# Performance work log

Measured on AMD Instinct MI355X. Metric: run time of the kernel, lower is better.

The kernel has to match this reference:

```python
import jax, jax.numpy as jnp
import numpy as np

B, N, C = 8, 4096, 1024
H = 16
D = C // H  # head_dim = 64
SCALE = D ** -0.5


def setup_inputs() -> dict:
    key = jax.random.key(0)
    ks = jax.random.split(key, 5)
    std = C ** -0.5
    return {
        "x": jax.random.normal(ks[0], (B, N, C), dtype=jnp.float32),
        "Wq": jax.random.normal(ks[1], (C, C), dtype=jnp.float32) * std,
        "Wk": jax.random.normal(ks[2], (C, C), dtype=jnp.float32) * std,
        "Wv": jax.random.normal(ks[3], (C, C), dtype=jnp.float32) * std,
        "Wo": jax.random.normal(ks[4], (C, C), dtype=jnp.float32) * std,
        "bo": jnp.zeros((C,), dtype=jnp.float32),
    }


def reference(x, Wq, Wk, Wv, Wo, bo):
    b, n, c = x.shape
    # projections -> (B, N, H, D)
    q = (x @ Wq).reshape(b, n, H, D)
    k = (x @ Wk).reshape(b, n, H, D)
    v = (x @ Wv).reshape(b, n, H, D)
    # feature maps: softmax over head_dim for q, over sequence for k
    q = jax.nn.softmax(q, axis=-1) * SCALE
    k = jax.nn.softmax(k, axis=1)
    # O(N) linear attention: kv summary then apply to q
    kv = jnp.einsum("bnhf,bnhd->bhfd", k, v)   # (B, H, D, D)
    y = jnp.einsum("bnhf,bhfd->bnhd", q, kv)   # (B, N, H, D)
    y = y.reshape(b, n, H * D)
    return y @ Wo + bo
```

## Files before the change

### kernel.cpp

```cpp
#include <hip/hip_runtime.h>


typedef unsigned short u16;
typedef __bf16 bf16x8v __attribute__((ext_vector_type(8)));
typedef float f32x4 __attribute__((ext_vector_type(4)));
typedef u16 u16x8 __attribute__((ext_vector_type(8)));
typedef u16 u16x4 __attribute__((ext_vector_type(4)));

#define AS1C(p) (const __attribute__((address_space(1))) void*)(p)
#define AS3(p)  (__attribute__((address_space(3))) void*)(p)

__device__ __forceinline__ float b2f(u16 u) {
    union { unsigned u; float f; } c; c.u = ((unsigned)u) << 16; return c.f;
}
__device__ __forceinline__ u16 f2b(float f) {
    union { float f; unsigned u; } c; c.f = f;
    unsigned x = c.u + 0x7fffu + ((c.u >> 16) & 1u);
    return (u16)(x >> 16);
}

__global__ void prep(const float* __restrict__ x, u16* __restrict__ xb,
                     const float* __restrict__ Wq, const float* __restrict__ Wk,
                     const float* __restrict__ Wv, const float* __restrict__ Wo,
                     u16* __restrict__ wt, u16* __restrict__ wot) {
    if (blockIdx.x < 1024) {
        __shared__ float tl[64][65];
        const int which = blockIdx.x >> 8;
        const float* src = which == 0 ? Wq : which == 1 ? Wk : which == 2 ? Wv : Wo;
        u16* dst = which < 3 ? wt + which * 1048576 : wot;
        const int bx = blockIdx.x & 255;
        const int tx = bx & 15, ty = bx >> 4;
        const int j = threadIdx.x & 63, i0 = threadIdx.x >> 6;
        #pragma unroll
        for (int it = 0; it < 16; ++it) {
            int i = it * 4 + i0;
            tl[i][j] = src[(ty * 64 + i) * 1024 + tx * 64 + j];
        }
        __syncthreads();
        #pragma unroll
        for (int it = 0; it < 16; ++it) {
            int i = it * 4 + i0;
            dst[(tx * 64 + i) * 1024 + ty * 64 + j] = f2b(tl[j][i]);
        }
    } else {
        const long n4 = 8388608L;
        long i = (long)(blockIdx.x - 1024) * blockDim.x + threadIdx.x;
        long stride = 2048L * blockDim.x;
        for (long jj = i; jj < n4; jj += stride) {
            float4 v = ((const float4*)x)[jj];
            u16x4 o = { f2b(v.x), f2b(v.y), f2b(v.z), f2b(v.w) };
            ((u16x4*)xb)[jj] = o;
        }
    }
}

template<int OUTMODE>
__global__ __launch_bounds__(512, 2) void gemm256(
    const u16* __restrict__ A, const u16* __restrict__ Bt,
    void* __restrict__ Cout, const float* __restrict__ bias,
    const int lda, const int ldc, const int ntn, const int nwg, const long btBatch)
{
    __shared__ __align__(16) u16 lds[65536];
    const int t = threadIdx.x;
    const int w = t >> 6, lane = t & 63;
    const int l16 = lane & 15, g = lane >> 4;
    const int wr = w >> 2, wc = w & 3;

    const int cpx = nwg >> 3;
    const int bid = blockIdx.x;
    const int swzb = (bid & 7) * cpx + (bid >> 3);
    const int tm = swzb / ntn, tn = swzb - tm * ntn;
    const long row0 = (long)tm << 8, col0 = (long)tn << 8;
    const u16* BtB = Bt + (row0 >> 12) * btBatch;

    const int eo = (((t & 7) ^ ((t >> 3) & 7)) << 3);
    const u16* pA = A + (row0 + (t >> 3)) * (long)lda + eo;
    const u16* pB = BtB + (col0 + (t >> 3)) * 1024L + eo;
    const long a64 = (long)lda << 6;

#define STG_A(Tt, j) __builtin_amdgcn_global_load_lds(                        \
    AS1C(pA + (long)(j) * a64 + ((long)(Tt) << 6)),                           \
    AS3(lds + ((((Tt) & 1) << 15) + ((j) << 12) + t * 8)), 16, 0, 0);
#define STG_B(Tt, j) __builtin_amdgcn_global_load_lds(                        \
    AS1C(pB + (long)(j) * 65536L + ((long)(Tt) << 6)),                        \
    AS3(lds + ((((Tt) & 1) << 15) + 16384 + ((j) << 12) + t * 8)), 16, 0, 0);

    const int swz = l16 & 7;
    const int koff0 = ((0 * 4 + g) ^ swz) << 3;
    const int koff1 = ((1 * 4 + g) ^ swz) << 3;
    const int arow = ((wr << 7) + l16) << 6;
    const int brow = 16384 + (((wc << 6) + l16) << 6);

    u16x8 aM[4][2], b0[2][2], b1[2][2];
    f32x4 acc[8][4] = {};

#define RD_A(half) { _Pragma("unroll") for (int mi = 0; mi < 4; ++mi) {       \
    const int ab = bufE + arow + ((half) * 64 + mi * 16) * 64;                \
    aM[mi][0] = *(const u16x8*)&lds[ab + koff0];                              \
    aM[mi][1] = *(const u16x8*)&lds[ab + koff1]; } }
#define RD_B(nh, br) { _Pragma("unroll") for (int ni = 0; ni < 2; ++ni) {     \
    const int bb = bufE + brow + ((nh) * 32 + ni * 16) * 64;                  \
    br[ni][0] = *(const u16x8*)&lds[bb + koff0];                              \
    br[ni][1] = *(const u16x8*)&lds[bb + koff1]; } }
#define MM(mh, nh, br) { __builtin_amdgcn_s_setprio(1);                       \
    _Pragma("unroll") for (int mi = 0; mi < 4; ++mi)                          \
    { _Pragma("unroll") for (int ni = 0; ni < 2; ++ni) {                      \
    f32x4 c = acc[(mh)*4 + mi][(nh)*2 + ni];                                  \
    c = __builtin_amdgcn_mfma_f32_16x16x32_bf16(                              \
        __builtin_bit_cast(bf16x8v, aM[mi][0]),                               \
        __builtin_bit_cast(bf16x8v, br[ni][0]), c, 0, 0, 0);                  \
    c = __builtin_amdgcn_mfma_f32_16x16x32_bf16(                              \
        __builtin_bit_cast(bf16x8v, aM[mi][1]),                               \
        __builtin_bit_cast(bf16x8v, br[ni][1]), c, 0, 0, 0);                  \
    acc[(mh)*4 + mi][(nh)*2 + ni] = c; } }                                    \
    __builtin_amdgcn_s_setprio(0); }

    STG_A(0, 0) STG_A(0, 2) STG_B(0, 0) STG_B(0, 1)
    STG_B(0, 2) STG_B(0, 3) STG_A(0, 1) STG_A(0, 3)
    STG_A(1, 0) STG_A(1, 2) STG_B(1, 0) STG_B(1, 1)
    asm volatile("s_waitcnt vmcnt(6)" ::: "memory");
    __builtin_amdgcn_s_barrier();

    #pragma unroll 2
    for (int T = 0; T < 16; ++T) {
        const int bufE = (T & 1) << 15;
        RD_A(0) RD_B(0, b0)
        STG_B(T + 1, 2) STG_B(T + 1, 3)
        __builtin_amdgcn_s_barrier();
        MM(0, 0, b0)
        RD_B(1, b1)
        STG_A(T + 1, 1) STG_A(T + 1, 3)
        asm volatile("s_waitcnt vmcnt(8)" ::: "memory");
        __builtin_amdgcn_s_barrier();
        MM(0, 1, b1)
        RD_A(1)
        STG_A(T + 2, 0) STG_A(T + 2, 2)
        __builtin_amdgcn_s_barrier();
        MM(1, 0, b0)
        STG_B(T + 2, 0) STG_B(T + 2, 1)
        asm volatile("s_waitcnt vmcnt(6)" ::: "memory");
        __builtin_amdgcn_s_barrier();
        MM(1, 1, b1)
    }
    asm volatile("s_waitcnt vmcnt(0)" ::: "memory");
#undef STG_A
#undef STG_B
#undef RD_A
#undef RD_B
#undef MM

    if (OUTMODE == 2 && tn < 4) {
        #pragma unroll
        for (int mi = 0; mi < 8; ++mi) {
            #pragma unroll
            for (int r = 0; r < 4; ++r) {
                float v0 = acc[mi][0][r], v1 = acc[mi][1][r];
                float v2 = acc[mi][2][r], v3 = acc[mi][3][r];
                float m = fmaxf(fmaxf(v0, v1), fmaxf(v2, v3));
                m = fmaxf(m, __shfl_xor(m, 1)); m = fmaxf(m, __shfl_xor(m, 2));
                m = fmaxf(m, __shfl_xor(m, 4)); m = fmaxf(m, __shfl_xor(m, 8));
                v0 = __expf(v0 - m); v1 = __expf(v1 - m);
                v2 = __expf(v2 - m); v3 = __expf(v3 - m);
                float s = v0 + v1 + v2 + v3;
                s += __shfl_xor(s, 1); s += __shfl_xor(s, 2);
                s += __shfl_xor(s, 4); s += __shfl_xor(s, 8);
                const float sc = 0.125f / s;
                acc[mi][0][r] = v0 * sc; acc[mi][1][r] = v1 * sc;
                acc[mi][2][r] = v2 * sc; acc[mi][3][r] = v3 * sc;
            }
        }
    }
    if (OUTMODE == 2 && tn >= 4 && tn < 8) {
        #pragma unroll
        for (int mi = 0; mi < 8; ++mi)
            #pragma unroll
            for (int ni = 0; ni < 4; ++ni)
                #pragma unroll
                for (int r = 0; r < 4; ++r)
                    acc[mi][ni][r] = __expf(acc[mi][ni][r]);
    }

    const long crow = row0 + wr * 128 + g * 4;
    const long ccol = col0 + wc * 64 + l16;
    if (OUTMODE != 1) {
        u16* Cb = (u16*)Cout;
        #pragma unroll
        for (int mi = 0; mi < 8; ++mi) {
            #pragma unroll
            for (int ni = 0; ni < 4; ++ni) {
                long base = (crow + mi * 16) * (long)ldc + ccol + ni * 16;
                #pragma unroll
                for (int r = 0; r < 4; ++r)
                    Cb[base + (long)r * ldc] = f2b(acc[mi][ni][r]);
            }
        }
    } else {
        float* Cf = (float*)Cout;
        float bv[4];
        #pragma unroll
        for (int ni = 0; ni < 4; ++ni) bv[ni] = bias[ccol + ni * 16];
        #pragma unroll
        for (int mi = 0; mi < 8; ++mi) {
            #pragma unroll
            for (int ni = 0; ni < 4; ++ni) {
                long base = (crow + mi * 16) * (long)ldc + ccol + ni * 16;
                #pragma unroll
                for (int r = 0; r < 4; ++r)
                    Cf[base + (long)r * ldc] = acc[mi][ni][r] + bv[ni];
            }
        }
    }
}

__global__ __launch_bounds__(256) void kv_mfma(const u16* __restrict__ qkv,
                                               float* __restrict__ kvp,
                                               float* __restrict__ psum) {
    __shared__ __align__(16) u16 eT[64 * 72];
    __shared__ __align__(16) u16 vT[64 * 72];
    __shared__ float csb[256 * 8];
    const int t = threadIdx.x;
    const int bx = blockIdx.x;
    const int nc = bx & 15, h = (bx >> 4) & 15, b = bx >> 8;
    const int r = t >> 3;
    const int c = t & 7;
    const long rowbase = (long)b * 4096 + nc * 256;
    const u16* eg = qkv + (rowbase + r) * 3072 + 1024 + h * 64 + c * 8;
    const u16* vg = eg + 1024;
    const int w = t >> 6, lane = t & 63;
    const int l16 = lane & 15, g = lane >> 4;

    float cs[8] = {};
    f32x4 acc[4] = {};

    int aoff[2], boff[4][2];
    #pragma unroll
    for (int ks = 0; ks < 2; ++ks) {
        const int f = w * 16 + l16;
        aoff[ks] = f * 72 + ((ks * 32 + g * 8) ^ (((f >> 3) & 7) << 3));
        #pragma unroll
        for (int db = 0; db < 4; ++db) {
            const int d = db * 16 + l16;
            boff[db][ks] = d * 72 + ((ks * 32 + g * 8) ^ (((d >> 3) & 7) << 3));
        }
    }

    for (int n0 = 0; n0 < 256; n0 += 64) {
        const long go = (long)n0 * 3072;
        u16x8 e0 = *(const u16x8*)(eg + go);
        u16x8 e1 = *(const u16x8*)(eg + go + 32L * 3072);
        u16x8 v0 = *(const u16x8*)(vg + go);
        u16x8 v1 = *(const u16x8*)(vg + go + 32L * 3072);
        #pragma unroll
        for (int j = 0; j < 8; ++j) {
            cs[j] += b2f(e0[j]) + b2f(e1[j]);
            const int f = c * 8 + j;
            const int sw = ((f >> 3) & 7) << 3;
            eT[f * 72 + (r ^ sw)]        = e0[j];
            eT[f * 72 + ((r + 32) ^ sw)] = e1[j];
            vT[f * 72 + (r ^ sw)]        = v0[j];
            vT[f * 72 + ((r + 32) ^ sw)] = v1[j];
        }
        __syncthreads();
        #pragma unroll
        for (int ks = 0; ks < 2; ++ks) {
            bf16x8v af = __builtin_bit_cast(bf16x8v, *(const u16x8*)&eT[aoff[ks]]);
            #pragma unroll
            for (int db = 0; db < 4; ++db) {
                bf16x8v bf = __builtin_bit_cast(bf16x8v, *(const u16x8*)&vT[boff[db][ks]]);
                acc[db] = __builtin_amdgcn_mfma_f32_16x16x32_bf16(af, bf, acc[db], 0, 0, 0);
            }
        }
        __syncthreads();
    }

    float* o = kvp + (long)nc * 524288 + ((long)(b * 16 + h)) * 4096;
    #pragma unroll
    for (int db = 0; db < 4; ++db) {
        #pragma unroll
        for (int rr = 0; rr < 4; ++rr)
            o[(w * 16 + g * 4 + rr) * 64 + db * 16 + l16] = acc[db][rr];
    }

    #pragma unroll
    for (int j = 0; j < 8; ++j) csb[t * 8 + j] = cs[j];
    __syncthreads();
    if (t < 64) {
        const int cc = t >> 3, jj = t & 7;
        float s = 0.f;
        #pragma unroll 8
        for (int rr = 0; rr < 32; ++rr) s += csb[(cc + 8 * rr) * 8 + jj];
        psum[((long)nc * 128 + b * 16 + h) * 64 + t] = s;
    }
}

__global__ void kv_scale(const float* __restrict__ kvp, const float* __restrict__ psum,
                         u16* __restrict__ kvNb) {
    __shared__ float inv_s[64];
    const int bh = blockIdx.x;
    const int t = threadIdx.x;
    if (t < 64) {
        float s = 0.f;
        #pragma unroll
        for (int nc = 0; nc < 16; ++nc) s += psum[((long)nc * 128 + bh) * 64 + t];
        inv_s[t] = 1.0f / s;
    }
    __syncthreads();
    const float* p = kvp + (long)bh * 4096;
    u16* o = kvNb + (long)bh * 4096;
    const float inv = inv_s[t >> 2];
    #pragma unroll
    for (int j = 0; j < 4; ++j) {
        const int idx = t * 16 + j * 4;
        f32x4 v = {};
        #pragma unroll
        for (int nc = 0; nc < 16; ++nc) {
            f32x4 pv = *(const f32x4*)&p[(long)nc * 524288 + idx];
            #pragma unroll
            for (int e = 0; e < 4; ++e) v[e] += pv[e];
        }
        u16x4 ov = { f2b(v[0] * inv), f2b(v[1] * inv), f2b(v[2] * inv), f2b(v[3] * inv) };
        *(u16x4*)&o[idx] = ov;
    }
}

__global__ __launch_bounds__(256) void w2t_mfma(const u16* __restrict__ wot,
                                                const u16* __restrict__ kvNb,
                                                u16* __restrict__ w2t) {
    __shared__ __align__(16) u16 Qs[8192];
    const int t = threadIdx.x;
    const int bx = blockIdx.x;
    const int mt = bx & 7, h = (bx >> 3) & 15, b = bx >> 7;
    const int c0 = mt * 128;
    const int wave = t >> 6, lane = t & 63;
    const int wr = wave >> 1, wc = wave & 1;
    const int l16 = lane & 15, g = lane >> 4;

    const int colg = t & 7;
    const int rloc = t >> 3;
    #pragma unroll
    for (int p = 0; p < 4; ++p) {
        const int row = p * 32 + rloc;
        u16x8 qv = *(const u16x8*)(wot + (long)(c0 + row) * 1024 + h * 64 + colg * 8);
        const int chunk = colg ^ (row & 7);
        *(u16x8*)&Qs[row * 64 + chunk * 8] = qv;
    }
    __syncthreads();

    const u16* kvb = kvNb + ((long)(b * 16 + h) << 12);
    bf16x8v bkv[2][2];
    #pragma unroll
    for (int ni = 0; ni < 2; ++ni) {
        #pragma unroll
        for (int ks = 0; ks < 2; ++ks)
            bkv[ni][ks] = __builtin_bit_cast(bf16x8v,
                *(const u16x8*)(kvb + (wc * 32 + ni * 16 + l16) * 64 + ks * 32 + g * 8));
    }
    bf16x8v aq[4][2];
    #pragma unroll
    for (int mi = 0; mi < 4; ++mi) {
        const int row = wr * 64 + mi * 16 + l16;
        #pragma unroll
        for (int ks = 0; ks < 2; ++ks) {
            const int c16 = (ks * 4 + g) ^ (row & 7);
            aq[mi][ks] = __builtin_bit_cast(bf16x8v,
                *(const u16x8*)&Qs[row * 64 + c16 * 8]);
        }
    }
    f32x4 acc[4][2] = {};
    #pragma unroll
    for (int mi = 0; mi < 4; ++mi) {
        #pragma unroll
        for (int ni = 0; ni < 2; ++ni) {
            acc[mi][ni] = __builtin_amdgcn_mfma_f32_16x16x32_bf16(
                aq[mi][0], bkv[ni][0], acc[mi][ni], 0, 0, 0);
            acc[mi][ni] = __builtin_amdgcn_mfma_f32_16x16x32_bf16(
                aq[mi][1], bkv[ni][1], acc[mi][ni], 0, 0, 0);
        }
    }
    u16* ob = w2t + (long)b * 1048576;
    #pragma unroll
    for (int mi = 0; mi < 4; ++mi) {
        #pragma unroll
        for (int ni = 0; ni < 2; ++ni) {
            int row = c0 + wr * 64 + mi * 16 + g * 4;
            int col = h * 64 + wc * 32 + ni * 16 + l16;
            #pragma unroll
            for (int r = 0; r < 4; ++r)
                ob[(long)(row + r) * 1024 + col] = f2b(acc[mi][ni][r]);
        }
    }
}

extern "C" void kernel_launch(void* const* d_in, const int* in_sizes, int n_in,
                              void* d_out, int out_size, void* d_ws, size_t ws_size,
                              hipStream_t stream) {
    (void)in_sizes; (void)n_in; (void)out_size; (void)ws_size;
    const float* x  = (const float*)d_in[0];
    const float* Wq = (const float*)d_in[1];
    const float* Wk = (const float*)d_in[2];
    const float* Wv = (const float*)d_in[3];
    const float* Wo = (const float*)d_in[4];
    const float* bo = (const float*)d_in[5];

    u16* xb  = (u16*)d_ws;
    u16* wt  = xb + 33554432;
    u16* wot = wt + 3145728;
    u16* qkv = wot + 1048576;
    u16* kvNb = qkv + 100663296;
    float* kvp  = (float*)xb;
    float* psum = kvp + 8388608;
    u16* w2t = (u16*)(psum + 131072);

    prep<<<3072, 256, 0, stream>>>(x, xb, Wq, Wk, Wv, Wo, wt, wot);
    gemm256<2><<<1536, 512, 0, stream>>>(xb, wt, (void*)qkv, nullptr, 1024, 3072, 12, 1536, 0L);
    kv_mfma<<<2048, 256, 0, stream>>>(qkv, kvp, psum);
    kv_scale<<<128, 256, 0, stream>>>(kvp, psum, kvNb);
    w2t_mfma<<<1024, 256, 0, stream>>>(wot, kvNb, w2t);
    gemm256<1><<<512, 512, 0, stream>>>(qkv, w2t, d_out, bo, 3072, 1024, 4, 512, 1048576L);
}
```

Measured before the change: 359.9 us.

## Fuse KV-summary computation into QKV projection GEMM epilogue

Reorders the K and V weight columns so each 256-wide output tile holds K and V for two heads. The QKV GEMM epilogue then computes exp(K), the per-chunk column sums and the K^T V partial products with MFMA through LDS. Only Q is written to global memory, which removes the K/V store plus the separate kv_mfma pass that read them back. The cost is a heavier epilogue with extra LDS round trips and barriers inside the GEMM kernel.

```diff
diff --git a/kernel.cpp b/kernel.cpp
--- a/kernel.cpp
+++ b/kernel.cpp
@@ -27,7 +27,6 @@
         __shared__ float tl[64][65];
         const int which = blockIdx.x >> 8;
         const float* src = which == 0 ? Wq : which == 1 ? Wk : which == 2 ? Wv : Wo;
-        u16* dst = which < 3 ? wt + which * 1048576 : wot;
         const int bx = blockIdx.x & 255;
         const int tx = bx & 15, ty = bx >> 4;
         const int j = threadIdx.x & 63, i0 = threadIdx.x >> 6;
@@ -40,7 +39,12 @@
         #pragma unroll
         for (int it = 0; it < 16; ++it) {
             int i = it * 4 + i0;
-            dst[(tx * 64 + i) * 1024 + ty * 64 + j] = f2b(tl[j][i]);
+            long row;
+            u16* base;
+            if (which == 0)      { base = wt;  row = tx * 64 + i; }
+            else if (which == 3) { base = wot; row = tx * 64 + i; }
+            else                 { base = wt;  row = 1024 + tx * 128 + (which == 2 ? 64 : 0) + i; }
+            base[row * 1024 + ty * 64 + j] = f2b(tl[j][i]);
         }
     } else {
         const long n4 = 8388608L;
@@ -58,7 +62,8 @@
 __global__ __launch_bounds__(512, 2) void gemm256(
     const u16* __restrict__ A, const u16* __restrict__ Bt,
     void* __restrict__ Cout, const float* __restrict__ bias,
-    const int lda, const int ldc, const int ntn, const int nwg, const long btBatch)
+    const int lda, const int ldc, const int ntn, const int nwg, const long btBatch,
+    float* __restrict__ kvp, float* __restrict__ psum)
 {
     __shared__ __align__(16) u16 lds[65536];
     const int t = threadIdx.x;
@@ -169,21 +174,9 @@
                 acc[mi][2][r] = v2 * sc; acc[mi][3][r] = v3 * sc;
             }
         }
-    }
-    if (OUTMODE == 2 && tn >= 4 && tn < 8) {
-        #pragma unroll
-        for (int mi = 0; mi < 8; ++mi)
-            #pragma unroll
-            for (int ni = 0; ni < 4; ++ni)
-                #pragma unroll
-                for (int r = 0; r < 4; ++r)
-                    acc[mi][ni][r] = __expf(acc[mi][ni][r]);
-    }
-
-    const long crow = row0 + wr * 128 + g * 4;
-    const long ccol = col0 + wc * 64 + l16;
-    if (OUTMODE != 1) {
         u16* Cb = (u16*)Cout;
+        const long crow = row0 + wr * 128 + g * 4;
+        const long ccol = col0 + wc * 64 + l16;
         #pragma unroll
         for (int mi = 0; mi < 8; ++mi) {
             #pragma unroll
@@ -194,8 +187,93 @@
                     Cb[base + (long)r * ldc] = f2b(acc[mi][ni][r]);
             }
         }
+    } else if (OUTMODE == 2) {
+        const int h0 = (tn - 4) * 2;
+        const int head = wc >> 1, kind = wc & 1;
+        const int bb = (int)(row0 >> 12);
+        const int nc = (int)((row0 >> 8) & 15);
+        float cs[4] = {};
+        if (kind == 0) {
+            #pragma unroll
+            for (int mi = 0; mi < 8; ++mi)
+                #pragma unroll
+                for (int ni = 0; ni < 4; ++ni)
+                    #pragma unroll
+                    for (int r = 0; r < 4; ++r) {
+                        float e = __expf(acc[mi][ni][r]);
+                        acc[mi][ni][r] = e;
+                        cs[ni] += e;
+                    }
+        }
+        f32x4 kvacc[4] = {};
+        const int myh = w >> 2, fb = w & 3;
+        const int frow = fb * 16 + l16;
+        const int aswz = frow & 0x38;
+        #pragma unroll
+        for (int p = 0; p < 4; ++p) {
+            __syncthreads();
+            if (wr == (p >> 1)) {
+                u16* dst = lds + (head * 2 + kind) * 4608;
+                #pragma unroll
+                for (int mi2 = 0; mi2 < 4; ++mi2) {
+                    #pragma unroll
+                    for (int r = 0; r < 4; ++r) {
+                        const int nl = mi2 * 16 + g * 4 + r;
+                        #pragma unroll
+                        for (int ni = 0; ni < 4; ++ni) {
+                            const int f = ni * 16 + l16;
+                            dst[f * 72 + (nl ^ (f & 0x38))] =
+                                f2b(acc[(p & 1) * 4 + mi2][ni][r]);
+                        }
+                    }
+                }
+            }
+            __syncthreads();
+            const u16* eB = lds + (myh * 2) * 4608;
+            const u16* vB = eB + 4608;
+            #pragma unroll
+            for (int ks = 0; ks < 2; ++ks) {
+                bf16x8v af = __builtin_bit_cast(bf16x8v,
+                    *(const u16x8*)&eB[frow * 72 + ((ks * 32 + g * 8) ^ aswz)]);
+                #pragma unroll
+                for (int db = 0; db < 4; ++db) {
+                    const int dr = db * 16 + l16;
+                    bf16x8v bf = __builtin_bit_cast(bf16x8v,
+                        *(const u16x8*)&vB[dr * 72 + ((ks * 32 + g * 8) ^ (dr & 0x38))]);
+                    kvacc[db] = __builtin_amdgcn_mfma_f32_16x16x32_bf16(
+                        af, bf, kvacc[db], 0, 0, 0);
+                }
+            }
+        }
+        float* o = kvp + (long)nc * 524288 + ((long)(bb * 16 + h0 + myh)) * 4096;
+        #pragma unroll
+        for (int db = 0; db < 4; ++db)
+            #pragma unroll
+            for (int rr = 0; rr < 4; ++rr)
+                o[(fb * 16 + g * 4 + rr) * 64 + db * 16 + l16] = kvacc[db][rr];
+        float* csb = (float*)(lds + 18432);
+        if (kind == 0) {
+            #pragma unroll
+            for (int ni = 0; ni < 4; ++ni) {
+                cs[ni] += __shfl_xor(cs[ni], 16);
+                cs[ni] += __shfl_xor(cs[ni], 32);
+            }
+            if (lane < 16) {
+                #pragma unroll
+                for (int ni = 0; ni < 4; ++ni)
+                    csb[(head * 2 + wr) * 64 + ni * 16 + lane] = cs[ni];
+            }
+        }
+        __syncthreads();
+        if (t < 128) {
+            const int hh = t >> 6, f = t & 63;
+            psum[((long)nc * 128 + bb * 16 + h0 + hh) * 64 + f] =
+                csb[(hh * 2) * 64 + f] + csb[(hh * 2 + 1) * 64 + f];
+        }
     } else {
         float* Cf = (float*)Cout;
+        const long crow = row0 + wr * 128 + g * 4;
+        const long ccol = col0 + wc * 64 + l16;
         float bv[4];
         #pragma unroll
         for (int ni = 0; ni < 4; ++ni) bv[ni] = bias[ccol + ni * 16];
@@ -209,87 +287,6 @@
                     Cf[base + (long)r * ldc] = acc[mi][ni][r] + bv[ni];
             }
         }
-    }
-}
-
-__global__ __launch_bounds__(256) void kv_mfma(const u16* __restrict__ qkv,
-                                               float* __restrict__ kvp,
-                                               float* __restrict__ psum) {
-    __shared__ __align__(16) u16 eT[64 * 72];
-    __shared__ __align__(16) u16 vT[64 * 72];
-    __shared__ float csb[256 * 8];
-    const int t = threadIdx.x;
-    const int bx = blockIdx.x;
-    const int nc = bx & 15, h = (bx >> 4) & 15, b = bx >> 8;
-    const int r = t >> 3;
-    const int c = t & 7;
-    const long rowbase = (long)b * 4096 + nc * 256;
-    const u16* eg = qkv + (rowbase + r) * 3072 + 1024 + h * 64 + c * 8;
-    const u16* vg = eg + 1024;
-    const int w = t >> 6, lane = t & 63;
-    const int l16 = lane & 15, g = lane >> 4;
-
-    float cs[8] = {};
-    f32x4 acc[4] = {};
-
-    int aoff[2], boff[4][2];
-    #pragma unroll
-    for (int ks = 0; ks < 2; ++ks) {
-        const int f = w * 16 + l16;
-        aoff[ks] = f * 72 + ((ks * 32 + g * 8) ^ (((f >> 3) & 7) << 3));
-        #pragma unroll
-        for (int db = 0; db < 4; ++db) {
-            const int d = db * 16 + l16;
-            boff[db][ks] = d * 72 + ((ks * 32 + g * 8) ^ (((d >> 3) & 7) << 3));
-        }
-    }
-
-    for (int n0 = 0; n0 < 256; n0 += 64) {
-        const long go = (long)n0 * 3072;
-        u16x8 e0 = *(const u16x8*)(eg + go);
-        u16x8 e1 = *(const u16x8*)(eg + go + 32L * 3072);
-        u16x8 v0 = *(const u16x8*)(vg + go);
-        u16x8 v1 = *(const u16x8*)(vg + go + 32L * 3072);
-        #pragma unroll
-        for (int j = 0; j < 8; ++j) {
-            cs[j] += b2f(e0[j]) + b2f(e1[j]);
-            const int f = c * 8 + j;
-            const int sw = ((f >> 3) & 7) << 3;
-            eT[f * 72 + (r ^ sw)]        = e0[j];
-            eT[f * 72 + ((r + 32) ^ sw)] = e1[j];
-            vT[f * 72 + (r ^ sw)]        = v0[j];
-            vT[f * 72 + ((r + 32) ^ sw)] = v1[j];
-        }
-        __syncthreads();
-        #pragma unroll
-        for (int ks = 0; ks < 2; ++ks) {
-            bf16x8v af = __builtin_bit_cast(bf16x8v, *(const u16x8*)&eT[aoff[ks]]);
-            #pragma unroll
-            for (int db = 0; db < 4; ++db) {
-                bf16x8v bf = __builtin_bit_cast(bf16x8v, *(const u16x8*)&vT[boff[db][ks]]);
-                acc[db] = __builtin_amdgcn_mfma_f32_16x16x32_bf16(af, bf, acc[db], 0, 0, 0);
-            }
-        }
-        __syncthreads();
-    }
-
-    float* o = kvp + (long)nc * 524288 + ((long)(b * 16 + h)) * 4096;
-    #pragma unroll
-    for (int db = 0; db < 4; ++db) {
-        #pragma unroll
-        for (int rr = 0; rr < 4; ++rr)
-            o[(w * 16 + g * 4 + rr) * 64 + db * 16 + l16] = acc[db][rr];
-    }
-
-    #pragma unroll
-    for (int j = 0; j < 8; ++j) csb[t * 8 + j] = cs[j];
-    __syncthreads();
-    if (t < 64) {
-        const int cc = t >> 3, jj = t & 7;
-        float s = 0.f;
-        #pragma unroll 8
-        for (int rr = 0; rr < 32; ++rr) s += csb[(cc + 8 * rr) * 8 + jj];
-        psum[((long)nc * 128 + b * 16 + h) * 64 + t] = s;
     }
 }
 
@@ -402,19 +399,20 @@
     const float* Wo = (const float*)d_in[4];
     const float* bo = (const float*)d_in[5];
 
-    u16* xb  = (u16*)d_ws;
-    u16* wt  = xb + 33554432;
-    u16* wot = wt + 3145728;
-    u16* qkv = wot + 1048576;
-    u16* kvNb = qkv + 100663296;
-    float* kvp  = (float*)xb;
+    u16* xb   = (u16*)d_ws;
+    u16* wt   = xb + 33554432;
+    u16* wot  = wt + 3145728;
+    u16* qkv  = wot + 1048576;
+    u16* kvNb = qkv + 33554432;
+    float* kvp  = (float*)(kvNb + 524288);
     float* psum = kvp + 8388608;
-    u16* w2t = (u16*)(psum + 131072);
+    u16* w2t  = (u16*)(psum + 131072);
 
     prep<<<3072, 256, 0, stream>>>(x, xb, Wq, Wk, Wv, Wo, wt, wot);
-    gemm256<2><<<1536, 512, 0, stream>>>(xb, wt, (void*)qkv, nullptr, 1024, 3072, 12, 1536, 0L);
-    kv_mfma<<<2048, 256, 0, stream>>>(qkv, kvp, psum);
+    gemm256<2><<<1536, 512, 0, stream>>>(xb, wt, (void*)qkv, nullptr,
+                                         1024, 1024, 12, 1536, 0L, kvp, psum);
     kv_scale<<<128, 256, 0, stream>>>(kvp, psum, kvNb);
     w2t_mfma<<<1024, 256, 0, stream>>>(wot, kvNb, w2t);
-    gemm256<1><<<512, 512, 0, stream>>>(qkv, w2t, d_out, bo, 3072, 1024, 4, 512, 1048576L);
-}
+    gemm256<1><<<512, 512, 0, stream>>>(qkv, w2t, d_out, bo,
+                                        1024, 1024, 4, 512, 1048576L, nullptr, nullptr);
+}
```

Measured after the change: 638.4 us. +77.4%, slower.
